# Optimization experiments

Hardware: AMD Instinct MI355X
Metric: run time of the kernel (lower is better)

Reference implementation:

```python
import jax, jax.numpy as jnp
import numpy as np

V = 50257   # vocab_size
D = 768     # d_model
NL = 4      # n_layers
DI = 1536   # d_inner = expand * d_model
DS = 16     # d_state
DC = 4      # d_conv
B = 2       # batch
L = 512     # seq_len
EPS = 1e-5  # RMSNorm eps
STD = 0.02  # init std


def setup_inputs() -> dict:
    key = jax.random.key(0)
    ks = jax.random.split(key, 8)
    idx = jax.random.randint(ks[0], (B, L), 0, V)
    emb = jax.random.normal(ks[1], (V, D), dtype=jnp.float32) * STD          # tied embedding / lm_head
    W_in = jax.random.normal(ks[2], (NL, 2 * DI, D), dtype=jnp.float32) * STD
    conv_w = jax.random.normal(ks[3], (NL, DI, 1, DC), dtype=jnp.float32) * STD  # depthwise conv [O,I/g,K]
    W_xproj = jax.random.normal(ks[4], (NL, 2 * DS + 1, DI), dtype=jnp.float32) * STD
    W_dt = jax.random.normal(ks[5], (NL, DI, 1), dtype=jnp.float32) * STD    # dt_rank = 1
    b_dt = jnp.zeros((NL, DI), dtype=jnp.float32)
    a_log = jnp.tile(jnp.log(jnp.arange(1, DS + 1, dtype=jnp.float32)), (NL, DI, 1))
    d_param = jnp.ones((NL, DI), dtype=jnp.float32)
    W_out = jax.random.normal(ks[6], (NL, D, DI), dtype=jnp.float32) * STD
    norm_w = jnp.ones((D,), dtype=jnp.float32)
    return dict(idx=idx, emb=emb, W_in=W_in, conv_w=conv_w, W_xproj=W_xproj,
                W_dt=W_dt, b_dt=b_dt, a_log=a_log, d_param=d_param,
                W_out=W_out, norm_w=norm_w)


def _mamba_block(x, W_in, conv_w, W_xproj, W_dt, b_dt, a_log, d_param, W_out):
    # in_proj + split into x, z
    xz = jnp.einsum('bld,ed->ble', x, W_in)            # [B,L,2*DI]
    xs, z = jnp.split(xz, 2, axis=-1)
    # causal depthwise conv1d (torch pads d_conv-1 both sides, keeps first L -> left pad only)
    xc = jnp.transpose(xs, (0, 2, 1))                  # [B,DI,L]
    xc = jax.lax.conv_general_dilated(xc, conv_w, window_strides=(1,),
                                      padding=[(DC - 1, 0)],
                                      feature_group_count=DI,
                                      dimension_numbers=('NCH', 'OIH', 'NCH'))
    xs = jax.nn.silu(jnp.transpose(xc, (0, 2, 1)))     # [B,L,DI]
    # selective SSM
    A = -jnp.exp(a_log)                                # [DI,DS]
    xp = jnp.einsum('bld,ed->ble', xs, W_xproj)        # [B,L,2*DS+1]
    dt_raw = xp[..., 0]                                # [B,L]
    Bp = xp[..., 1:1 + DS]                             # [B,L,DS]
    Cp = xp[..., 1 + DS:]                              # [B,L,DS]
    delta = jax.nn.softplus(dt_raw[..., None] * W_dt[:, 0] + b_dt)  # [B,L,DI]

    def step(h, inp):
        d_i, b_i, c_i, x_i = inp                       # [B,DI],[B,DS],[B,DS],[B,DI]
        a_bar = jnp.exp(d_i[:, :, None] * A)           # [B,DI,DS]
        h = a_bar * h + d_i[:, :, None] * b_i[:, None, :] * x_i[:, :, None]
        y = jnp.einsum('bn,bdn->bd', c_i, h) + d_param * x_i
        return h, y

    h0 = jnp.zeros((x.shape[0], DI, DS), dtype=x.dtype)
    seq = (jnp.moveaxis(delta, 1, 0), jnp.moveaxis(Bp, 1, 0),
           jnp.moveaxis(Cp, 1, 0), jnp.moveaxis(xs, 1, 0))
    _, ys = jax.lax.scan(step, h0, seq)
    y = jnp.moveaxis(ys, 0, 1)                         # [B,L,DI]
    y = y * jax.nn.silu(z)
    return jnp.einsum('ble,de->bld', y, W_out)         # [B,L,D]


def reference(idx, emb, W_in, conv_w, W_xproj, W_dt, b_dt, a_log, d_param, W_out, norm_w):
    x = emb[idx]                                       # [B,L,D]

    def layer(carry, p):
        w_in, c_w, w_xp, w_dt, bdt, alog, dpar, w_out = p
        out = carry + _mamba_block(carry, w_in, c_w, w_xp, w_dt, bdt, alog, dpar, w_out)
        return out, None

    x, _ = jax.lax.scan(layer, x, (W_in, conv_w, W_xproj, W_dt, b_dt, a_log, d_param, W_out))
    rms = jax.lax.rsqrt(jnp.mean(x * x, axis=-1, keepdims=True) + EPS)
    x = x * rms * norm_w
    logits = jnp.einsum('bld,vd->blv', x, emb)         # tied lm_head
    return logits
```

## Files before the change

kernel.cpp:

```cpp
#include <hip/hip_runtime.h>
#include <cstdint>

#define VV     50257
#define VPAD   50432
#define DMODEL 768
#define NLAYER 4
#define DINNER 1536
#define DSTATE 16
#define DCONV  4
#define BATCH  2
#define SEQ    512
#define MROWS  (BATCH*SEQ)

typedef unsigned short u16;
typedef __attribute__((ext_vector_type(8))) short bf16x8;
typedef __attribute__((ext_vector_type(4))) float f32x4;

__device__ __forceinline__ u16 f2bf(float f) {
  unsigned u = __float_as_uint(f);
  u += 0x7fffu + ((u >> 16) & 1u);
  return (u16)(u >> 16);
}

__device__ __forceinline__ void async16(const void* g, void* l) {
  auto gp = reinterpret_cast<const __attribute__((address_space(1))) unsigned int*>(
      reinterpret_cast<uintptr_t>(g));
  auto lp = reinterpret_cast<__attribute__((address_space(3))) unsigned int*>(
      reinterpret_cast<uintptr_t>(l));
  __builtin_amdgcn_global_load_lds(gp, lp, 16, 0, 0);
}

__global__ void prep_kern(const float* __restrict__ emb, const float* __restrict__ W_in,
                          const float* __restrict__ W_out, const int* __restrict__ idx,
                          u16* __restrict__ embbf, u16* __restrict__ winbf,
                          u16* __restrict__ woutbf, float* __restrict__ xf,
                          u16* __restrict__ xbf) {
  const int E4  = VPAD * DMODEL / 4;
  const int W14 = NLAYER * 2 * DINNER * DMODEL / 4;
  const int W24 = NLAYER * DMODEL * DINNER / 4;
  const int X4  = MROWS * DMODEL / 4;
  const int TOT = E4 + W14 + W24 + X4;
  int i = blockIdx.x * blockDim.x + threadIdx.x;
  const int stride = gridDim.x * blockDim.x;
  for (; i < TOT; i += stride) {
    if (i < E4) {
      ushort4 o;
      if (i < VV * DMODEL / 4) {
        float4 v = *(const float4*)(emb + (long)i * 4);
        o.x = f2bf(v.x); o.y = f2bf(v.y); o.z = f2bf(v.z); o.w = f2bf(v.w);
      } else { o.x = 0; o.y = 0; o.z = 0; o.w = 0; }
      *(ushort4*)(embbf + (long)i * 4) = o;
    } else if (i < E4 + W14) {
      const int j = i - E4;
      float4 v = *(const float4*)(W_in + (long)j * 4);
      ushort4 o; o.x = f2bf(v.x); o.y = f2bf(v.y); o.z = f2bf(v.z); o.w = f2bf(v.w);
      *(ushort4*)(winbf + (long)j * 4) = o;
    } else if (i < E4 + W14 + W24) {
      const int j = i - E4 - W14;
      float4 v = *(const float4*)(W_out + (long)j * 4);
      ushort4 o; o.x = f2bf(v.x); o.y = f2bf(v.y); o.z = f2bf(v.z); o.w = f2bf(v.w);
      *(ushort4*)(woutbf + (long)j * 4) = o;
    } else {
      const int j = i - E4 - W14 - W24;
      const int r = j / (DMODEL / 4);
      const int c = (j % (DMODEL / 4)) * 4;
      const int id = idx[r];
      float4 v = *(const float4*)(emb + (long)id * DMODEL + c);
      *(float4*)(xf + (long)r * DMODEL + c) = v;
      ushort4 o; o.x = f2bf(v.x); o.y = f2bf(v.y); o.z = f2bf(v.z); o.w = f2bf(v.w);
      *(ushort4*)(xbf + (long)r * DMODEL + c) = o;
    }
  }
}

template<bool GUARDN, bool XSWZ>
__global__ __launch_bounds__(256) void gemm3_kern(
    const u16* __restrict__ A, const u16* __restrict__ B,
    float* __restrict__ C, int M, int N, int K, int lda, int ldb)
{
  __shared__ u16 As[3][128 * 32];
  __shared__ u16 Bs[3][128 * 32];
  int bx, by;
  if (XSWZ) {
    const int nt = gridDim.x >> 3;
    const int t = (blockIdx.x & 7) * nt + (blockIdx.x >> 3);
    bx = t & 7; by = t >> 3;
  } else { bx = blockIdx.x; by = blockIdx.y; }
  const int koff = blockIdx.z * K;
  const long coff = (long)blockIdx.z * M * N;

  const int tid  = threadIdx.x;
  const int wave = tid >> 6;
  const int lane = tid & 63;
  const int wr = wave >> 1, wc = wave & 1;
  const int m0 = bx * 128;
  const int n0 = by * 128;

  const int srow = wave * 32 + (lane >> 2);
  const int sblk = ((lane & 3) ^ ((lane >> 3) & 3)) * 8;

  f32x4 acc[4][4];
#pragma unroll
  for (int i = 0; i < 4; ++i)
#pragma unroll
    for (int j = 0; j < 4; ++j) acc[i][j] = (f32x4){0.f, 0.f, 0.f, 0.f};

  const int arow = wr * 64 + (lane & 15);
  const int brow = wc * 64 + (lane & 15);
  const int sa   = (((lane >> 4) ^ ((lane >> 1) & 3)) << 3);

  const int KT = K / 32;
  auto stage = [&](int kt) {
    const int slot = kt % 3;
    const long kcol = (long)koff + kt * 32;
#pragma unroll
    for (int j = 0; j < 2; ++j) {
      async16(A + (long)(m0 + srow + j * 16) * lda + kcol + sblk,
              (char*)(As[slot]) + (wave * 32 + j * 16) * 64);
      async16(B + (long)(n0 + srow + j * 16) * ldb + kcol + sblk,
              (char*)(Bs[slot]) + (wave * 32 + j * 16) * 64);
    }
  };

  stage(0);
  stage(1);
  for (int t = 0; t < KT; ++t) {
    if (t + 2 < KT) {
      stage(t + 2);
      asm volatile("s_waitcnt vmcnt(8)" ::: "memory");
    } else if (t + 2 == KT) {
      asm volatile("s_waitcnt vmcnt(4)" ::: "memory");
    } else {
      asm volatile("s_waitcnt vmcnt(0)" ::: "memory");
    }
    __builtin_amdgcn_s_barrier();
    asm volatile("" ::: "memory");

    const int slot = t % 3;
    const u16* as = As[slot];
    const u16* bs = Bs[slot];
    bf16x8 af[4], bv[4];
#pragma unroll
    for (int i = 0; i < 4; ++i) af[i] = *(const bf16x8*)(as + (arow + 16 * i) * 32 + sa);
#pragma unroll
    for (int j = 0; j < 4; ++j) bv[j] = *(const bf16x8*)(bs + (brow + 16 * j) * 32 + sa);

    __builtin_amdgcn_s_setprio(1);
#pragma unroll
    for (int i = 0; i < 4; ++i)
#pragma unroll
      for (int j = 0; j < 4; ++j)
        acc[i][j] = __builtin_amdgcn_mfma_f32_16x16x32_bf16(af[i], bv[j], acc[i][j], 0, 0, 0);
    __builtin_amdgcn_s_setprio(0);

    asm volatile("" ::: "memory");
    __builtin_amdgcn_s_barrier();
    asm volatile("" ::: "memory");
  }

  const int rbase = m0 + wr * 64 + ((lane >> 4) << 2);
  const int cbase = n0 + wc * 64 + (lane & 15);
#pragma unroll
  for (int j = 0; j < 4; ++j) {
    const int col = cbase + j * 16;
    if (GUARDN && col >= N) continue;
#pragma unroll
    for (int i = 0; i < 4; ++i) {
#pragma unroll
      for (int r = 0; r < 4; ++r) {
        const int row = rbase + i * 16 + r;
        C[coff + (long)row * N + col] = acc[i][j][r];
      }
    }
  }
}

__global__ __launch_bounds__(512, 2) void gemm8_kern(
    const u16* __restrict__ A, const u16* __restrict__ B,
    float* __restrict__ C, int N, int K, int lda, int ldb)
{
  __shared__ u16 lds[2][2][256 * 64];
  const int tid = threadIdx.x;
  const int wave = tid >> 6;
  const int lane = tid & 63;
  const int wm = wave >> 2, wn = wave & 3;

  const int nwg = gridDim.x;
  const int q = nwg >> 3, r = nwg & 7;
  const int xcd = blockIdx.x & 7;
  const int t = (xcd < r ? xcd * (q + 1) : r * (q + 1) + (xcd - r) * q) + (blockIdx.x >> 3);
  const int m0 = (t & 3) * 256;
  const int n0 = (t >> 2) * 256;

  const int NT = K / 64;

  const int sblk = (((lane & 7) ^ (lane >> 3)) << 3);
  auto stage = [&](int buf, int ab, int half, int kt) {
    const u16* Mat = ab ? B : A;
    const int ld = ab ? ldb : lda;
    const int tb = ab ? n0 : m0;
#pragma unroll
    for (int j = 0; j < 2; ++j) {
      const int rloc = half * 128 + j * 64 + wave * 8;
      async16(Mat + (long)(tb + rloc + (lane >> 3)) * ld + kt * 64 + sblk,
              (char*)&lds[buf][ab][0] + (rloc << 7));
    }
  };

  bf16x8 af[4][2], bl[2][2], bh[2][2];
  const int aq = lane >> 4;
  auto readA = [&](int buf, int half) {
#pragma unroll
    for (int mf = 0; mf < 4; ++mf) {
      const int rr = half * 128 + wm * 64 + mf * 16 + (lane & 15);
#pragma unroll
      for (int ks = 0; ks < 2; ++ks) {
        const int q2 = ks * 4 + aq;
        af[mf][ks] = *(const bf16x8*)(&lds[buf][0][0] + rr * 64 + ((q2 ^ (rr & 7)) << 3));
      }
    }
  };
  auto readB = [&](int buf, int half, bf16x8 (&bf)[2][2]) {
#pragma unroll
    for (int nf = 0; nf < 2; ++nf) {
      const int rr = half * 128 + wn * 32 + nf * 16 + (lane & 15);
#pragma unroll
      for (int ks = 0; ks < 2; ++ks) {
        const int q2 = ks * 4 + aq;
        bf[nf][ks] = *(const bf16x8*)(&lds[buf][1][0] + rr * 64 + ((q2 ^ (rr & 7)) << 3));
      }
    }
  };

  f32x4 acc[8][4];
#pragma unroll
  for (int i = 0; i < 8; ++i)
#pragma unroll
    for (int j = 0; j < 4; ++j) acc[i][j] = (f32x4){0.f, 0.f, 0.f, 0.f};

#define MFMA16(QM, QN, BF)                                                        \
  __builtin_amdgcn_s_setprio(1);                                                  \
  _Pragma("unroll")                                                               \
  for (int mf = 0; mf < 4; ++mf)                                                  \
    _Pragma("unroll")                                                             \
    for (int nf = 0; nf < 2; ++nf)                                                \
      _Pragma("unroll")                                                           \
      for (int ks = 0; ks < 2; ++ks)                                              \
        acc[(QM)*4+mf][(QN)*2+nf] = __builtin_amdgcn_mfma_f32_16x16x32_bf16(      \
            af[mf][ks], BF[nf][ks], acc[(QM)*4+mf][(QN)*2+nf], 0, 0, 0);          \
  __builtin_amdgcn_s_setprio(0);

#define BAR()   asm volatile("" ::: "memory"); __builtin_amdgcn_s_barrier(); asm volatile("" ::: "memory")
#define WAITV(N) asm volatile("s_waitcnt vmcnt(" #N ")" ::: "memory"); __builtin_amdgcn_sched_barrier(0)
#define WAITL(N) asm volatile("s_waitcnt lgkmcnt(" #N ")" ::: "memory"); __builtin_amdgcn_sched_barrier(0)

  stage(0, 0, 0, 0); stage(0, 1, 0, 0); stage(0, 1, 1, 0); stage(0, 0, 1, 0);
  stage(1, 0, 0, 1); stage(1, 1, 0, 1); stage(1, 1, 1, 1);
  WAITV(6);
  BAR();
  readB(0, 0, bl);

#define TILE(KTE, BUF)                                                            \
  {                                                                               \
    const int kt = (KTE);                                                         \
                                                               \
    if (kt >= NT - 2) { WAITV(0); } else { WAITV(8); }                            \
    BAR();                                                                        \
    readA(BUF, 0);                                          \
    readB(BUF, 1, bh);                            \
    if (kt + 1 < NT) stage(BUF ^ 1, 0, 1, kt + 1);                  \
    WAITL(4);                                  \
    MFMA16(0, 0, bl);                                                             \
                                                               \
    BAR();                                                                        \
    if (kt + 2 < NT) stage(BUF, 0, 0, kt + 2);                      \
    WAITL(0);                                                      \
    MFMA16(0, 1, bh);                                                             \
                                                               \
    if (kt >= NT - 2) { WAITV(0); } else { WAITV(10); }                           \
    BAR();                                                                        \
    readA(BUF, 1);                           \
    if (kt + 2 < NT) stage(BUF, 1, 0, kt + 2);                      \
    WAITL(0);                                                     \
    MFMA16(1, 0, bl);                                                             \
                                                               \
    if (kt >= NT - 2) { WAITV(0); } else { WAITV(8); }                            \
    BAR();                                                                        \
    if (kt + 1 < NT) readB(BUF ^ 1, 0, bl);               \
    if (kt + 2 < NT) stage(BUF, 1, 1, kt + 2);                      \
    WAITL(4);                                      \
    MFMA16(1, 1, bh);                                                             \
  }

  for (int kt2 = 0; kt2 < NT; kt2 += 2) {
    TILE(kt2, 0);
    TILE(kt2 + 1, 1);
  }

#pragma unroll
  for (int qm = 0; qm < 2; ++qm)
#pragma unroll
    for (int mf = 0; mf < 4; ++mf)
#pragma unroll
      for (int qn = 0; qn < 2; ++qn)
#pragma unroll
        for (int nf = 0; nf < 2; ++nf) {
          const int col = n0 + qn * 128 + wn * 32 + nf * 16 + (lane & 15);
          if (col >= N) continue;
          const int row0 = m0 + qm * 128 + wm * 64 + mf * 16 + ((lane >> 4) << 2);
          const f32x4 v = acc[qm * 4 + mf][qn * 2 + nf];
#pragma unroll
          for (int rr2 = 0; rr2 < 4; ++rr2)
            C[(long)(row0 + rr2) * N + col] = v[rr2];
        }
#undef TILE
#undef MFMA16
#undef BAR
#undef WAITV
#undef WAITL
}

__global__ __launch_bounds__(256) void redout_kern(const float* __restrict__ part,
                                                   float* __restrict__ xf,
                                                   u16* __restrict__ xbf) {
  const int i = blockIdx.x * blockDim.x + threadIdx.x;
  if (i >= MROWS * DMODEL / 4) return;
  const int stride4 = MROWS * DMODEL / 4;
  float4 s = ((const float4*)part)[i];
  float4 p1 = ((const float4*)part)[i + stride4];
  float4 p2 = ((const float4*)part)[i + 2 * stride4];
  float4 p3 = ((const float4*)part)[i + 3 * stride4];
  float4 x = ((const float4*)xf)[i];
  s.x += p1.x + p2.x + p3.x + x.x;
  s.y += p1.y + p2.y + p3.y + x.y;
  s.z += p1.z + p2.z + p3.z + x.z;
  s.w += p1.w + p2.w + p3.w + x.w;
  ((float4*)xf)[i] = s;
  ushort4 o; o.x = f2bf(s.x); o.y = f2bf(s.y); o.z = f2bf(s.z); o.w = f2bf(s.w);
  ((ushort4*)xbf)[i] = o;
}

__global__ __launch_bounds__(256) void convxproj_kern(
    const float* __restrict__ xz, const float* __restrict__ cw,
    const float* __restrict__ Wx, const float* __restrict__ wdt,
    const float* __restrict__ bdt,
    float* __restrict__ xs, float* __restrict__ dlt, float* __restrict__ bc)
{
  __shared__ float sx[DINNER];
  __shared__ float sxp[40];
  const int row = blockIdx.x;
  const int t = row & (SEQ - 1);
  const int tid = threadIdx.x;

  for (int c = tid; c < DINNER; c += 256) {
    const float* w = cw + c * DCONV;
    float a = 0.f;
#pragma unroll
    for (int k = 0; k < DCONV; ++k) {
      const int tt = t - (DCONV - 1) + k;
      if (tt >= 0) a += w[k] * xz[(long)(row - (DCONV - 1) + k) * (2 * DINNER) + c];
    }
    const float s = a / (1.f + __expf(-a));
    sx[c] = s;
    xs[(long)row * DINNER + c] = s;
  }
  __syncthreads();

  const int wv = tid >> 6, lane = tid & 63;
  for (int e = wv; e < 2 * DSTATE + 1; e += 4) {
    const float* We = Wx + (long)e * DINNER;
    float p = 0.f;
    for (int d = lane; d < DINNER; d += 64) p += sx[d] * We[d];
#pragma unroll
    for (int off = 32; off; off >>= 1) p += __shfl_xor(p, off, 64);
    if (lane == 0) sxp[e] = p;
  }
  __syncthreads();
  const float dtr = sxp[0];
  for (int d = tid; d < DINNER; d += 256) {
    float v = dtr * wdt[d] + bdt[d];
    float sp = (v > 15.f) ? v : log1pf(__expf(v));
    dlt[(long)row * DINNER + d] = sp;
  }
  if (tid < 2 * DSTATE) bc[(long)row * (2 * DSTATE) + tid] = sxp[1 + tid];
}

__global__ __launch_bounds__(128) void scan_kern(
    const float* __restrict__ dlt, const float* __restrict__ bc,
    const float* __restrict__ xs, const float* __restrict__ xz,
    const float* __restrict__ alog, const float* __restrict__ dpar,
    u16* __restrict__ ybf)
{
  __shared__ float sh_h[16][8][DSTATE];
  __shared__ float sh_s[16][8];
  const int tid = threadIdx.x;
  const int ch = tid & 7, chunk = tid >> 3;
  const int ch_abs = blockIdx.x * 8 + ch;
  const int b = ch_abs / DINNER, d = ch_abs % DINNER;
  float An[DSTATE];
#pragma unroll
  for (int n = 0; n < DSTATE; ++n) An[n] = -__expf(alog[(long)d * DSTATE + n]);
  const int r0 = b * SEQ + chunk * 32;

  float h[DSTATE];
#pragma unroll
  for (int n = 0; n < DSTATE; ++n) h[n] = 0.f;
  float ssum = 0.f;
  for (int s = 0; s < 32; ++s) {
    const int row = r0 + s;
    const float dl = dlt[(long)row * DINNER + d];
    const float xv = xs[(long)row * DINNER + d];
    const float dx = dl * xv;
    const float4* bp = (const float4*)(bc + (long)row * (2 * DSTATE));
    float Bv[DSTATE];
    *(float4*)&Bv[0]  = bp[0]; *(float4*)&Bv[4]  = bp[1];
    *(float4*)&Bv[8]  = bp[2]; *(float4*)&Bv[12] = bp[3];
    ssum += dl;
#pragma unroll
    for (int n = 0; n < DSTATE; ++n) h[n] = __expf(dl * An[n]) * h[n] + dx * Bv[n];
  }
#pragma unroll
  for (int n = 0; n < DSTATE; ++n) sh_h[chunk][ch][n] = h[n];
  sh_s[chunk][ch] = ssum;
  __syncthreads();

  {
    const int n2 = tid & 15, ch2 = tid >> 4;
    const int d2 = (blockIdx.x * 8 + ch2) % DINNER;
    const float A2 = -__expf(alog[(long)d2 * DSTATE + n2]);
    float carry = 0.f;
    for (int c = 0; c < 16; ++c) {
      const float hl = sh_h[c][ch2][n2];
      sh_h[c][ch2][n2] = carry;
      carry = __expf(A2 * sh_s[c][ch2]) * carry + hl;
    }
  }
  __syncthreads();

#pragma unroll
  for (int n = 0; n < DSTATE; ++n) h[n] = sh_h[chunk][ch][n];
  const float dp = dpar[d];
  for (int s = 0; s < 32; ++s) {
    const int row = r0 + s;
    const float dl = dlt[(long)row * DINNER + d];
    const float xv = xs[(long)row * DINNER + d];
    const float dx = dl * xv;
    const float4* bp = (const float4*)(bc + (long)row * (2 * DSTATE));
    float Bv[DSTATE], Cv[DSTATE];
    *(float4*)&Bv[0]  = bp[0]; *(float4*)&Bv[4]  = bp[1];
    *(float4*)&Bv[8]  = bp[2]; *(float4*)&Bv[12] = bp[3];
    *(float4*)&Cv[0]  = bp[4]; *(float4*)&Cv[4]  = bp[5];
    *(float4*)&Cv[8]  = bp[6]; *(float4*)&Cv[12] = bp[7];
    float y = 0.f;
#pragma unroll
    for (int n = 0; n < DSTATE; ++n) {
      const float hn = __expf(dl * An[n]) * h[n] + dx * Bv[n];
      h[n] = hn;
      y += Cv[n] * hn;
    }
    y += dp * xv;
    const float zz = xz[(long)row * (2 * DINNER) + DINNER + d];
    const float o = y * (zz / (1.f + __expf(-zz)));
    ybf[(long)row * DINNER + d] = f2bf(o);
  }
}

__global__ __launch_bounds__(256) void rmsfuse_kern(const float* __restrict__ part,
                                                    const float* __restrict__ xf,
                                                    const float* __restrict__ nw,
                                                    u16* __restrict__ xnbf) {
  const int row = blockIdx.x, tid = threadIdx.x;
  const int S = MROWS * DMODEL;
  float v[3];
  float p = 0.f;
#pragma unroll
  for (int k = 0; k < 3; ++k) {
    const int i = row * DMODEL + tid + k * 256;
    float x = xf[i] + part[i] + part[i + S] + part[i + 2 * S] + part[i + 3 * S];
    v[k] = x;
    p += x * x;
  }
#pragma unroll
  for (int off = 32; off; off >>= 1) p += __shfl_xor(p, off, 64);
  __shared__ float red[4];
  __shared__ float s_rms;
  const int wv = tid >> 6, lane = tid & 63;
  if (lane == 0) red[wv] = p;
  __syncthreads();
  if (tid == 0) {
    float tsum = red[0] + red[1] + red[2] + red[3];
    s_rms = rsqrtf(tsum / (float)DMODEL + 1e-5f);
  }
  __syncthreads();
  const float r = s_rms;
#pragma unroll
  for (int k = 0; k < 3; ++k) {
    const int dd = tid + k * 256;
    xnbf[(long)row * DMODEL + dd] = f2bf(v[k] * r * nw[dd]);
  }
}

extern "C" void kernel_launch(void* const* d_in, const int* in_sizes, int n_in,
                              void* d_out, int out_size, void* d_ws, size_t ws_size,
                              hipStream_t stream)
{
  (void)in_sizes; (void)n_in; (void)out_size; (void)ws_size;
  const int*   idx   = (const int*)  d_in[0];
  const float* emb   = (const float*)d_in[1];
  const float* W_in  = (const float*)d_in[2];
  const float* convw = (const float*)d_in[3];
  const float* W_xp  = (const float*)d_in[4];
  const float* W_dt  = (const float*)d_in[5];
  const float* b_dt  = (const float*)d_in[6];
  const float* a_log = (const float*)d_in[7];
  const float* d_par = (const float*)d_in[8];
  const float* W_out = (const float*)d_in[9];
  const float* normw = (const float*)d_in[10];
  float* out = (float*)d_out;

  char* ws = (char*)d_ws;
  size_t off = 0;
  auto alloc = [&](size_t bytes) -> void* {
    void* p = ws + off;
    off += (bytes + 255) & ~(size_t)255;
    return p;
  };
  u16*   embbf  = (u16*)  alloc((size_t)VPAD * DMODEL * 2);
  u16*   winbf  = (u16*)  alloc((size_t)NLAYER * 2 * DINNER * DMODEL * 2);
  u16*   woutbf = (u16*)  alloc((size_t)NLAYER * DMODEL * DINNER * 2);
  float* xf     = (float*)alloc((size_t)MROWS * DMODEL * 4);
  u16*   xbf    = (u16*)  alloc((size_t)MROWS * DMODEL * 2);
  float* xz     = (float*)alloc((size_t)MROWS * 2 * DINNER * 4);
  float* xs     = (float*)alloc((size_t)MROWS * DINNER * 4);
  float* dlt    = (float*)alloc((size_t)MROWS * DINNER * 4);
  float* bc     = (float*)alloc((size_t)MROWS * 2 * DSTATE * 4);
  u16*   ybf    = (u16*)  alloc((size_t)MROWS * DINNER * 2);
  u16*   xnbf   = (u16*)  alloc((size_t)MROWS * DMODEL * 2);
  float* part   = (float*)alloc((size_t)4 * MROWS * DMODEL * 4);

  prep_kern<<<2048, 256, 0, stream>>>(emb, W_in, W_out, idx, embbf, winbf, woutbf, xf, xbf);

  for (int l = 0; l < NLAYER; ++l) {
    gemm3_kern<false, true><<<8 * (2 * DINNER / 128), 256, 0, stream>>>(
        xbf, winbf + (size_t)l * 2 * DINNER * DMODEL, xz,
        MROWS, 2 * DINNER, DMODEL, DMODEL, DMODEL);
    convxproj_kern<<<MROWS, 256, 0, stream>>>(
        xz, convw + (size_t)l * DINNER * DCONV,
        W_xp + (size_t)l * (2 * DSTATE + 1) * DINNER,
        W_dt + (size_t)l * DINNER, b_dt + (size_t)l * DINNER, xs, dlt, bc);
    scan_kern<<<BATCH * DINNER / 8, 128, 0, stream>>>(
        dlt, bc, xs, xz, a_log + (size_t)l * DINNER * DSTATE, d_par + (size_t)l * DINNER, ybf);
    gemm3_kern<false, true><<<dim3(8 * (DMODEL / 128), 1, 4), 256, 0, stream>>>(
        ybf, woutbf + (size_t)l * DMODEL * DINNER, part,
        MROWS, DMODEL, DINNER / 4, DINNER, DINNER);
    if (l < NLAYER - 1)
      redout_kern<<<MROWS * DMODEL / 4 / 256, 256, 0, stream>>>(part, xf, xbf);
  }
  rmsfuse_kern<<<MROWS, 256, 0, stream>>>(part, xf, normw, xnbf);
  gemm8_kern<<<4 * (VPAD / 256), 512, 0, stream>>>(
      xnbf, embbf, out, VV, DMODEL, DMODEL, DMODEL);
}
```

Baseline: 883.5 us.

## Make the lm_head GEMM persistent with a simple double-buffered pipeline

Replaces the one-tile-per-block lm_head GEMM with a persistent kernel of 256 blocks. Each block loops over its share of XCD-grouped 256x256 output tiles and prefetches the first k-tile of the next output tile before running the epilogue store. The finely interleaved half-tile stage/read/MFMA schedule is replaced by a plain two-buffer loop with one barrier pair per k-tile. The aim is to cut launch/tail overhead and overlap output stores with the next tile's loads, but it gives up the finer LDS/MFMA overlap of the old schedule.

```diff
diff --git a/kernel.cpp b/kernel.cpp
--- a/kernel.cpp
+++ b/kernel.cpp
@@ -136,9 +136,8 @@
     __builtin_amdgcn_s_barrier();
     asm volatile("" ::: "memory");
 
-    const int slot = t % 3;
-    const u16* as = As[slot];
-    const u16* bs = Bs[slot];
+    const u16* as = As[t % 3];
+    const u16* bs = Bs[t % 3];
     bf16x8 af[4], bv[4];
 #pragma unroll
     for (int i = 0; i < 4; ++i) af[i] = *(const bf16x8*)(as + (arow + 16 * i) * 32 + sa);
@@ -175,7 +174,7 @@
   }
 }
 
-__global__ __launch_bounds__(512, 2) void gemm8_kern(
+__global__ __launch_bounds__(512, 2) void gemm8p_kern(
     const u16* __restrict__ A, const u16* __restrict__ B,
     float* __restrict__ C, int N, int K, int lda, int ldb)
 {
@@ -184,35 +183,35 @@
   const int wave = tid >> 6;
   const int lane = tid & 63;
   const int wm = wave >> 2, wn = wave & 3;
-
-  const int nwg = gridDim.x;
-  const int q = nwg >> 3, r = nwg & 7;
+  const int NT = K / 64;
+
   const int xcd = blockIdx.x & 7;
-  const int t = (xcd < r ? xcd * (q + 1) : r * (q + 1) + (xcd - r) * q) + (blockIdx.x >> 3);
-  const int m0 = (t & 3) * 256;
-  const int n0 = (t >> 2) * 256;
-
-  const int NT = K / 64;
+  const int lin = blockIdx.x >> 3;
+  const int NTILES = 4 * (VPAD / 256);
+  const int qq = NTILES / 8, rr8 = NTILES % 8;
+  const int cnt = qq + (xcd < rr8 ? 1 : 0);
+  const int base = xcd * qq + (xcd < rr8 ? xcd : rr8);
 
   const int sblk = (((lane & 7) ^ (lane >> 3)) << 3);
-  auto stage = [&](int buf, int ab, int half, int kt) {
-    const u16* Mat = ab ? B : A;
-    const int ld = ab ? ldb : lda;
-    const int tb = ab ? n0 : m0;
-#pragma unroll
-    for (int j = 0; j < 2; ++j) {
-      const int rloc = half * 128 + j * 64 + wave * 8;
-      async16(Mat + (long)(tb + rloc + (lane >> 3)) * ld + kt * 64 + sblk,
-              (char*)&lds[buf][ab][0] + (rloc << 7));
-    }
+  auto stage = [&](int buf, int kt, int m0, int n0) {
+#pragma unroll
+    for (int half = 0; half < 2; ++half)
+#pragma unroll
+      for (int j = 0; j < 2; ++j) {
+        const int rloc = half * 128 + j * 64 + wave * 8;
+        async16(A + (long)(m0 + rloc + (lane >> 3)) * lda + kt * 64 + sblk,
+                (char*)&lds[buf][0][0] + (rloc << 7));
+        async16(B + (long)(n0 + rloc + (lane >> 3)) * ldb + kt * 64 + sblk,
+                (char*)&lds[buf][1][0] + (rloc << 7));
+      }
   };
 
-  bf16x8 af[4][2], bl[2][2], bh[2][2];
   const int aq = lane >> 4;
-  auto readA = [&](int buf, int half) {
+  bf16x8 af[4][2], bb[4][2];
+  auto readA = [&](int buf, int qm) {
 #pragma unroll
     for (int mf = 0; mf < 4; ++mf) {
-      const int rr = half * 128 + wm * 64 + mf * 16 + (lane & 15);
+      const int rr = qm * 128 + wm * 64 + mf * 16 + (lane & 15);
 #pragma unroll
       for (int ks = 0; ks < 2; ++ks) {
         const int q2 = ks * 4 + aq;
@@ -220,104 +219,107 @@
       }
     }
   };
-  auto readB = [&](int buf, int half, bf16x8 (&bf)[2][2]) {
-#pragma unroll
-    for (int nf = 0; nf < 2; ++nf) {
-      const int rr = half * 128 + wn * 32 + nf * 16 + (lane & 15);
-#pragma unroll
-      for (int ks = 0; ks < 2; ++ks) {
-        const int q2 = ks * 4 + aq;
-        bf[nf][ks] = *(const bf16x8*)(&lds[buf][1][0] + rr * 64 + ((q2 ^ (rr & 7)) << 3));
+  auto readB = [&](int buf) {
+#pragma unroll
+    for (int qn = 0; qn < 2; ++qn)
+#pragma unroll
+      for (int nf = 0; nf < 2; ++nf) {
+        const int rr = qn * 128 + wn * 32 + nf * 16 + (lane & 15);
+#pragma unroll
+        for (int ks = 0; ks < 2; ++ks) {
+          const int q2 = ks * 4 + aq;
+          bb[qn * 2 + nf][ks] = *(const bf16x8*)(&lds[buf][1][0] + rr * 64 + ((q2 ^ (rr & 7)) << 3));
+        }
       }
-    }
   };
 
-  f32x4 acc[8][4];
-#pragma unroll
-  for (int i = 0; i < 8; ++i)
-#pragma unroll
-    for (int j = 0; j < 4; ++j) acc[i][j] = (f32x4){0.f, 0.f, 0.f, 0.f};
-
-#define MFMA16(QM, QN, BF)                                                        \
-  __builtin_amdgcn_s_setprio(1);                                                  \
-  _Pragma("unroll")                                                               \
-  for (int mf = 0; mf < 4; ++mf)                                                  \
-    _Pragma("unroll")                                                             \
-    for (int nf = 0; nf < 2; ++nf)                                                \
-      _Pragma("unroll")                                                           \
-      for (int ks = 0; ks < 2; ++ks)                                              \
-        acc[(QM)*4+mf][(QN)*2+nf] = __builtin_amdgcn_mfma_f32_16x16x32_bf16(      \
-            af[mf][ks], BF[nf][ks], acc[(QM)*4+mf][(QN)*2+nf], 0, 0, 0);          \
-  __builtin_amdgcn_s_setprio(0);
-
-#define BAR()   asm volatile("" ::: "memory"); __builtin_amdgcn_s_barrier(); asm volatile("" ::: "memory")
-#define WAITV(N) asm volatile("s_waitcnt vmcnt(" #N ")" ::: "memory"); __builtin_amdgcn_sched_barrier(0)
-#define WAITL(N) asm volatile("s_waitcnt lgkmcnt(" #N ")" ::: "memory"); __builtin_amdgcn_sched_barrier(0)
-
-  stage(0, 0, 0, 0); stage(0, 1, 0, 0); stage(0, 1, 1, 0); stage(0, 0, 1, 0);
-  stage(1, 0, 0, 1); stage(1, 1, 0, 1); stage(1, 1, 1, 1);
-  WAITV(6);
-  BAR();
-  readB(0, 0, bl);
-
-#define TILE(KTE, BUF)                                                            \
-  {                                                                               \
-    const int kt = (KTE);                                                         \
-                                                               \
-    if (kt >= NT - 2) { WAITV(0); } else { WAITV(8); }                            \
-    BAR();                                                                        \
-    readA(BUF, 0);                                          \
-    readB(BUF, 1, bh);                            \
-    if (kt + 1 < NT) stage(BUF ^ 1, 0, 1, kt + 1);                  \
-    WAITL(4);                                  \
-    MFMA16(0, 0, bl);                                                             \
-                                                               \
-    BAR();                                                                        \
-    if (kt + 2 < NT) stage(BUF, 0, 0, kt + 2);                      \
-    WAITL(0);                                                      \
-    MFMA16(0, 1, bh);                                                             \
-                                                               \
-    if (kt >= NT - 2) { WAITV(0); } else { WAITV(10); }                           \
-    BAR();                                                                        \
-    readA(BUF, 1);                           \
-    if (kt + 2 < NT) stage(BUF, 1, 0, kt + 2);                      \
-    WAITL(0);                                                     \
-    MFMA16(1, 0, bl);                                                             \
-                                                               \
-    if (kt >= NT - 2) { WAITV(0); } else { WAITV(8); }                            \
-    BAR();                                                                        \
-    if (kt + 1 < NT) readB(BUF ^ 1, 0, bl);               \
-    if (kt + 2 < NT) stage(BUF, 1, 1, kt + 2);                      \
-    WAITL(4);                                      \
-    MFMA16(1, 1, bh);                                                             \
-  }
-
-  for (int kt2 = 0; kt2 < NT; kt2 += 2) {
-    TILE(kt2, 0);
-    TILE(kt2 + 1, 1);
-  }
-
-#pragma unroll
-  for (int qm = 0; qm < 2; ++qm)
-#pragma unroll
-    for (int mf = 0; mf < 4; ++mf)
-#pragma unroll
-      for (int qn = 0; qn < 2; ++qn)
-#pragma unroll
-        for (int nf = 0; nf < 2; ++nf) {
-          const int col = n0 + qn * 128 + wn * 32 + nf * 16 + (lane & 15);
-          if (col >= N) continue;
-          const int row0 = m0 + qm * 128 + wm * 64 + mf * 16 + ((lane >> 4) << 2);
-          const f32x4 v = acc[qm * 4 + mf][qn * 2 + nf];
-#pragma unroll
-          for (int rr2 = 0; rr2 < 4; ++rr2)
-            C[(long)(row0 + rr2) * N + col] = v[rr2];
-        }
-#undef TILE
-#undef MFMA16
-#undef BAR
+#define WAITV(NN) asm volatile("s_waitcnt vmcnt(" #NN ")" ::: "memory"); __builtin_amdgcn_sched_barrier(0)
+#define WAITL0()  asm volatile("s_waitcnt lgkmcnt(0)" ::: "memory"); __builtin_amdgcn_sched_barrier(0)
+
+  bool first = true;
+  for (int u = base + lin; u < base + cnt; u += 32) {
+    const int m0 = (u & 3) * 256;
+    const int n0 = (u >> 2) * 256;
+
+    f32x4 acc[8][4];
+#pragma unroll
+    for (int i = 0; i < 8; ++i)
+#pragma unroll
+      for (int j = 0; j < 4; ++j) acc[i][j] = (f32x4){0.f, 0.f, 0.f, 0.f};
+
+    if (first) { stage(0, 0, m0, n0); first = false; }
+
+    for (int kt = 0; kt < NT; ++kt) {
+      const int buf = kt & 1;
+      if (kt + 1 < NT) {
+        stage(buf ^ 1, kt + 1, m0, n0);
+        WAITV(8);
+      } else {
+        WAITV(0);
+      }
+      __builtin_amdgcn_s_barrier();
+      asm volatile("" ::: "memory");
+
+      readB(buf);
+      readA(buf, 0);
+      WAITL0();
+      __builtin_amdgcn_s_setprio(1);
+#pragma unroll
+      for (int mf = 0; mf < 4; ++mf)
+#pragma unroll
+        for (int qn = 0; qn < 2; ++qn)
+#pragma unroll
+          for (int nf = 0; nf < 2; ++nf)
+#pragma unroll
+            for (int ks = 0; ks < 2; ++ks)
+              acc[mf][qn * 2 + nf] = __builtin_amdgcn_mfma_f32_16x16x32_bf16(
+                  af[mf][ks], bb[qn * 2 + nf][ks], acc[mf][qn * 2 + nf], 0, 0, 0);
+      __builtin_amdgcn_s_setprio(0);
+
+      readA(buf, 1);
+      WAITL0();
+      __builtin_amdgcn_s_setprio(1);
+#pragma unroll
+      for (int mf = 0; mf < 4; ++mf)
+#pragma unroll
+        for (int qn = 0; qn < 2; ++qn)
+#pragma unroll
+          for (int nf = 0; nf < 2; ++nf)
+#pragma unroll
+            for (int ks = 0; ks < 2; ++ks)
+              acc[4 + mf][qn * 2 + nf] = __builtin_amdgcn_mfma_f32_16x16x32_bf16(
+                  af[mf][ks], bb[qn * 2 + nf][ks], acc[4 + mf][qn * 2 + nf], 0, 0, 0);
+      __builtin_amdgcn_s_setprio(0);
+
+      asm volatile("" ::: "memory");
+      __builtin_amdgcn_s_barrier();
+      asm volatile("" ::: "memory");
+    }
+
+    const int un = u + 32;
+    if (un < base + cnt) {
+      stage(0, 0, (un & 3) * 256, (un >> 2) * 256);
+    }
+
+#pragma unroll
+    for (int qm = 0; qm < 2; ++qm)
+#pragma unroll
+      for (int mf = 0; mf < 4; ++mf)
+#pragma unroll
+        for (int qn = 0; qn < 2; ++qn)
+#pragma unroll
+          for (int nf = 0; nf < 2; ++nf) {
+            const int col = n0 + qn * 128 + wn * 32 + nf * 16 + (lane & 15);
+            if (col >= N) continue;
+            const int row0 = m0 + qm * 128 + wm * 64 + mf * 16 + ((lane >> 4) << 2);
+            const f32x4 v = acc[qm * 4 + mf][qn * 2 + nf];
+#pragma unroll
+            for (int rr2 = 0; rr2 < 4; ++rr2)
+              C[(long)(row0 + rr2) * N + col] = v[rr2];
+          }
+  }
 #undef WAITV
-#undef WAITL
+#undef WAITL0
 }
 
 __global__ __launch_bounds__(256) void redout_kern(const float* __restrict__ part,
@@ -557,6 +559,6 @@
       redout_kern<<<MROWS * DMODEL / 4 / 256, 256, 0, stream>>>(part, xf, xbf);
   }
   rmsfuse_kern<<<MROWS, 256, 0, stream>>>(part, xf, normw, xnbf);
-  gemm8_kern<<<4 * (VPAD / 256), 512, 0, stream>>>(
+  gemm8p_kern<<<256, 512, 0, stream>>>(
       xnbf, embbf, out, VV, DMODEL, DMODEL, DMODEL);
 }
```

After: 905.9 us. 1.03x slower.

## Split-K the in_proj GEMM and deepen scan chunk parallelism

Applied to the files above, without the earlier changes.

The in_proj GEMM now runs split-K by two over the grid z dimension, writing two partial xz buffers. The conv and scan kernels sum those partials when they read xz. The scan kernel also doubles its chunks per block, from 16 chunks of 32 steps to 32 chunks of 16 steps, with 256 threads. The aim is more parallelism for a small GEMM grid and for the sequential scan, at the cost of extra xz memory traffic and a longer carry-propagation loop.

```diff
diff --git a/kernel.cpp b/kernel.cpp
--- a/kernel.cpp
+++ b/kernel.cpp
@@ -11,6 +11,7 @@
 #define BATCH  2
 #define SEQ    512
 #define MROWS  (BATCH*SEQ)
+#define XZS    ((long)MROWS * 2 * DINNER)
 
 typedef unsigned short u16;
 typedef __attribute__((ext_vector_type(8))) short bf16x8;
@@ -136,9 +137,8 @@
     __builtin_amdgcn_s_barrier();
     asm volatile("" ::: "memory");
 
-    const int slot = t % 3;
-    const u16* as = As[slot];
-    const u16* bs = Bs[slot];
+    const u16* as = As[t % 3];
+    const u16* bs = Bs[t % 3];
     bf16x8 af[4], bv[4];
 #pragma unroll
     for (int i = 0; i < 4; ++i) af[i] = *(const bf16x8*)(as + (arow + 16 * i) * 32 + sa);
@@ -251,8 +251,8 @@
   __builtin_amdgcn_s_setprio(0);
 
 #define BAR()   asm volatile("" ::: "memory"); __builtin_amdgcn_s_barrier(); asm volatile("" ::: "memory")
-#define WAITV(N) asm volatile("s_waitcnt vmcnt(" #N ")" ::: "memory"); __builtin_amdgcn_sched_barrier(0)
-#define WAITL(N) asm volatile("s_waitcnt lgkmcnt(" #N ")" ::: "memory"); __builtin_amdgcn_sched_barrier(0)
+#define WAITV(NN) asm volatile("s_waitcnt vmcnt(" #NN ")" ::: "memory"); __builtin_amdgcn_sched_barrier(0)
+#define WAITL(NN) asm volatile("s_waitcnt lgkmcnt(" #NN ")" ::: "memory"); __builtin_amdgcn_sched_barrier(0)
 
   stage(0, 0, 0, 0); stage(0, 1, 0, 0); stage(0, 1, 1, 0); stage(0, 0, 1, 0);
   stage(1, 0, 0, 1); stage(1, 1, 0, 1); stage(1, 1, 1, 1);
@@ -263,32 +263,28 @@
 #define TILE(KTE, BUF)                                                            \
   {                                                                               \
     const int kt = (KTE);                                                         \
-                                                               \
     if (kt >= NT - 2) { WAITV(0); } else { WAITV(8); }                            \
     BAR();                                                                        \
-    readA(BUF, 0);                                          \
-    readB(BUF, 1, bh);                            \
-    if (kt + 1 < NT) stage(BUF ^ 1, 0, 1, kt + 1);                  \
-    WAITL(4);                                  \
+    readA(BUF, 0);                                                                \
+    readB(BUF, 1, bh);                                                            \
+    if (kt + 1 < NT) stage(BUF ^ 1, 0, 1, kt + 1);                                \
+    WAITL(4);                                                                     \
     MFMA16(0, 0, bl);                                                             \
-                                                               \
     BAR();                                                                        \
-    if (kt + 2 < NT) stage(BUF, 0, 0, kt + 2);                      \
-    WAITL(0);                                                      \
+    if (kt + 2 < NT) stage(BUF, 0, 0, kt + 2);                                    \
+    WAITL(0);                                                                     \
     MFMA16(0, 1, bh);                                                             \
-                                                               \
     if (kt >= NT - 2) { WAITV(0); } else { WAITV(10); }                           \
     BAR();                                                                        \
-    readA(BUF, 1);                           \
-    if (kt + 2 < NT) stage(BUF, 1, 0, kt + 2);                      \
-    WAITL(0);                                                     \
+    readA(BUF, 1);                                                                \
+    if (kt + 2 < NT) stage(BUF, 1, 0, kt + 2);                                    \
+    WAITL(0);                                                                     \
     MFMA16(1, 0, bl);                                                             \
-                                                               \
     if (kt >= NT - 2) { WAITV(0); } else { WAITV(8); }                            \
     BAR();                                                                        \
-    if (kt + 1 < NT) readB(BUF ^ 1, 0, bl);               \
-    if (kt + 2 < NT) stage(BUF, 1, 1, kt + 2);                      \
-    WAITL(4);                                      \
+    if (kt + 1 < NT) readB(BUF ^ 1, 0, bl);                                       \
+    if (kt + 2 < NT) stage(BUF, 1, 1, kt + 2);                                    \
+    WAITL(4);                                                                     \
     MFMA16(1, 1, bh);                                                             \
   }
 
@@ -358,7 +354,10 @@
 #pragma unroll
     for (int k = 0; k < DCONV; ++k) {
       const int tt = t - (DCONV - 1) + k;
-      if (tt >= 0) a += w[k] * xz[(long)(row - (DCONV - 1) + k) * (2 * DINNER) + c];
+      if (tt >= 0) {
+        const long ix = (long)(row - (DCONV - 1) + k) * (2 * DINNER) + c;
+        a += w[k] * (xz[ix] + xz[ix + XZS]);
+      }
     }
     const float s = a / (1.f + __expf(-a));
     sx[c] = s;
@@ -385,14 +384,14 @@
   if (tid < 2 * DSTATE) bc[(long)row * (2 * DSTATE) + tid] = sxp[1 + tid];
 }
 
-__global__ __launch_bounds__(128) void scan_kern(
+__global__ __launch_bounds__(256) void scan_kern(
     const float* __restrict__ dlt, const float* __restrict__ bc,
     const float* __restrict__ xs, const float* __restrict__ xz,
     const float* __restrict__ alog, const float* __restrict__ dpar,
     u16* __restrict__ ybf)
 {
-  __shared__ float sh_h[16][8][DSTATE];
-  __shared__ float sh_s[16][8];
+  __shared__ float sh_h[32][8][DSTATE];
+  __shared__ float sh_s[32][8];
   const int tid = threadIdx.x;
   const int ch = tid & 7, chunk = tid >> 3;
   const int ch_abs = blockIdx.x * 8 + ch;
@@ -400,21 +399,21 @@
   float An[DSTATE];
 #pragma unroll
   for (int n = 0; n < DSTATE; ++n) An[n] = -__expf(alog[(long)d * DSTATE + n]);
-  const int r0 = b * SEQ + chunk * 32;
+  const int r0 = b * SEQ + chunk * 16;
 
   float h[DSTATE];
 #pragma unroll
   for (int n = 0; n < DSTATE; ++n) h[n] = 0.f;
   float ssum = 0.f;
-  for (int s = 0; s < 32; ++s) {
+  for (int s = 0; s < 16; ++s) {
     const int row = r0 + s;
     const float dl = dlt[(long)row * DINNER + d];
     const float xv = xs[(long)row * DINNER + d];
     const float dx = dl * xv;
     const float4* bp = (const float4*)(bc + (long)row * (2 * DSTATE));
     float Bv[DSTATE];
-    *(float4*)&Bv[0]  = bp[0]; *(float4*)&Bv[4]  = bp[1];
-    *(float4*)&Bv[8]  = bp[2]; *(float4*)&Bv[12] = bp[3];
+    *(float4*)&Bv[0] = bp[0]; *(float4*)&Bv[4] = bp[1];
+    *(float4*)&Bv[8] = bp[2]; *(float4*)&Bv[12] = bp[3];
     ssum += dl;
 #pragma unroll
     for (int n = 0; n < DSTATE; ++n) h[n] = __expf(dl * An[n]) * h[n] + dx * Bv[n];
@@ -424,12 +423,12 @@
   sh_s[chunk][ch] = ssum;
   __syncthreads();
 
-  {
+  if (tid < 128) {
     const int n2 = tid & 15, ch2 = tid >> 4;
     const int d2 = (blockIdx.x * 8 + ch2) % DINNER;
     const float A2 = -__expf(alog[(long)d2 * DSTATE + n2]);
     float carry = 0.f;
-    for (int c = 0; c < 16; ++c) {
+    for (int c = 0; c < 32; ++c) {
       const float hl = sh_h[c][ch2][n2];
       sh_h[c][ch2][n2] = carry;
       carry = __expf(A2 * sh_s[c][ch2]) * carry + hl;
@@ -440,17 +439,17 @@
 #pragma unroll
   for (int n = 0; n < DSTATE; ++n) h[n] = sh_h[chunk][ch][n];
   const float dp = dpar[d];
-  for (int s = 0; s < 32; ++s) {
+  for (int s = 0; s < 16; ++s) {
     const int row = r0 + s;
     const float dl = dlt[(long)row * DINNER + d];
     const float xv = xs[(long)row * DINNER + d];
     const float dx = dl * xv;
     const float4* bp = (const float4*)(bc + (long)row * (2 * DSTATE));
     float Bv[DSTATE], Cv[DSTATE];
-    *(float4*)&Bv[0]  = bp[0]; *(float4*)&Bv[4]  = bp[1];
-    *(float4*)&Bv[8]  = bp[2]; *(float4*)&Bv[12] = bp[3];
-    *(float4*)&Cv[0]  = bp[4]; *(float4*)&Cv[4]  = bp[5];
-    *(float4*)&Cv[8]  = bp[6]; *(float4*)&Cv[12] = bp[7];
+    *(float4*)&Bv[0] = bp[0]; *(float4*)&Bv[4] = bp[1];
+    *(float4*)&Bv[8] = bp[2]; *(float4*)&Bv[12] = bp[3];
+    *(float4*)&Cv[0] = bp[4]; *(float4*)&Cv[4] = bp[5];
+    *(float4*)&Cv[8] = bp[6]; *(float4*)&Cv[12] = bp[7];
     float y = 0.f;
 #pragma unroll
     for (int n = 0; n < DSTATE; ++n) {
@@ -459,7 +458,8 @@
       y += Cv[n] * hn;
     }
     y += dp * xv;
-    const float zz = xz[(long)row * (2 * DINNER) + DINNER + d];
+    const long zix = (long)row * (2 * DINNER) + DINNER + d;
+    const float zz = xz[zix] + xz[zix + XZS];
     const float o = y * (zz / (1.f + __expf(-zz)));
     ybf[(long)row * DINNER + d] = f2bf(o);
   }
@@ -530,7 +530,7 @@
   u16*   woutbf = (u16*)  alloc((size_t)NLAYER * DMODEL * DINNER * 2);
   float* xf     = (float*)alloc((size_t)MROWS * DMODEL * 4);
   u16*   xbf    = (u16*)  alloc((size_t)MROWS * DMODEL * 2);
-  float* xz     = (float*)alloc((size_t)MROWS * 2 * DINNER * 4);
+  float* xz     = (float*)alloc((size_t)2 * MROWS * 2 * DINNER * 4);
   float* xs     = (float*)alloc((size_t)MROWS * DINNER * 4);
   float* dlt    = (float*)alloc((size_t)MROWS * DINNER * 4);
   float* bc     = (float*)alloc((size_t)MROWS * 2 * DSTATE * 4);
@@ -541,14 +541,14 @@
   prep_kern<<<2048, 256, 0, stream>>>(emb, W_in, W_out, idx, embbf, winbf, woutbf, xf, xbf);
 
   for (int l = 0; l < NLAYER; ++l) {
-    gemm3_kern<false, true><<<8 * (2 * DINNER / 128), 256, 0, stream>>>(
+    gemm3_kern<false, true><<<dim3(8 * (2 * DINNER / 128), 1, 2), 256, 0, stream>>>(
         xbf, winbf + (size_t)l * 2 * DINNER * DMODEL, xz,
-        MROWS, 2 * DINNER, DMODEL, DMODEL, DMODEL);
+        MROWS, 2 * DINNER, DMODEL / 2, DMODEL, DMODEL);
     convxproj_kern<<<MROWS, 256, 0, stream>>>(
         xz, convw + (size_t)l * DINNER * DCONV,
         W_xp + (size_t)l * (2 * DSTATE + 1) * DINNER,
         W_dt + (size_t)l * DINNER, b_dt + (size_t)l * DINNER, xs, dlt, bc);
-    scan_kern<<<BATCH * DINNER / 8, 128, 0, stream>>>(
+    scan_kern<<<BATCH * DINNER / 8, 256, 0, stream>>>(
         dlt, bc, xs, xz, a_log + (size_t)l * DINNER * DSTATE, d_par + (size_t)l * DINNER, ybf);
     gemm3_kern<false, true><<<dim3(8 * (DMODEL / 128), 1, 4), 256, 0, stream>>>(
         ybf, woutbf + (size_t)l * DMODEL * DINNER, part,
```

New measurement: 794.5 us. 1.11x faster.
